# Kernel optimization log

Hardware: AMD Instinct MI355X
Metric: run time of the kernel (lower is better)

The kernel has to match this reference:

```python
import jax, jax.numpy as jnp
import numpy as np

N_STUDENT = 100000
N_COURSE = 20000
N_EDGES = 1000000
HIDDEN = 128


def setup_inputs() -> dict:
    key = jax.random.key(0)
    ks = jax.random.split(key, 8)
    scale = 1.0 / np.sqrt(2 * HIDDEN)
    return {
        "z_student": jax.random.normal(ks[0], (N_STUDENT, HIDDEN), dtype=jnp.float32),
        "z_course": jax.random.normal(ks[1], (N_COURSE, HIDDEN), dtype=jnp.float32),
        "row": jax.random.randint(ks[2], (N_EDGES,), 0, N_STUDENT, dtype=jnp.int64),
        "col": jax.random.randint(ks[3], (N_EDGES,), 0, N_COURSE, dtype=jnp.int64),
        "W1": jax.random.normal(ks[4], (2 * HIDDEN, HIDDEN), dtype=jnp.float32) * scale,
        "b1": jnp.zeros((HIDDEN,), dtype=jnp.float32),
        "W2": jax.random.normal(ks[5], (HIDDEN, 1), dtype=jnp.float32) * (1.0 / np.sqrt(HIDDEN)),
        "b2": jnp.zeros((1,), dtype=jnp.float32),
    }


def reference(z_student, z_course, row, col, W1, b1, W2, b2):
    # gather endpoint embeddings and concat along feature dim: [E, 2H]
    z = jnp.concatenate([z_student[row], z_course[col]], axis=-1)
    h = jax.nn.relu(z @ W1 + b1)   # [E, H]
    out = h @ W2 + b2              # [E, 1]
    return out.reshape(-1)
```

## Files before the change

kernel.cpp:

```cpp
#include <hip/hip_runtime.h>
#include <hip/hip_bf16.h>
#include <hip/hip_fp16.h>


typedef _Float16 half2v __attribute__((ext_vector_type(2)));
typedef _Float16 half8v __attribute__((ext_vector_type(8)));
typedef __fp16   fp16x2 __attribute__((ext_vector_type(2)));
typedef float    float4v __attribute__((ext_vector_type(4)));

__global__ __launch_bounds__(256) void conv_w(const float* __restrict__ W1,
                                              const float* __restrict__ W2,
                                              _Float16* __restrict__ Wt,
                                              _Float16* __restrict__ w2h) {
    int b = blockIdx.x, t = threadIdx.x;
    if (b == 8) { if (t < 128) w2h[t] = (_Float16)W2[t]; return; }
    __shared__ _Float16 lds[32][136];
    int h = b >> 2, n0 = (b & 3) * 32;
    for (int i = 0; i < 16; ++i) {
        int idx = i * 256 + t;
        int k = idx >> 5, nn = idx & 31;
        lds[nn][k] = (_Float16)W1[(h * 128 + k) * 128 + n0 + nn];
    }
    __syncthreads();
    for (int j = 0; j < 2; ++j) {
        int idx = j * 256 + t;
        int nn = idx >> 4, kc = idx & 15;
        half8v v;
        #pragma unroll
        for (int q = 0; q < 8; ++q) v[q] = lds[nn][kc * 8 + q];
        *(half8v*)&Wt[((h * 128 + n0 + nn) * 128) + kc * 8] = v;
    }
}

__global__ __launch_bounds__(256) void gemm_u(
    const float* __restrict__ Zs, const float* __restrict__ Zc,
    const _Float16* __restrict__ Wt, const float* __restrict__ b1,
    _Float16* __restrict__ Us, _Float16* __restrict__ Uc,
    int Ms, int Mc, int nbs)
{
    __shared__ uint4 ldsW[2048];
    const int bid = blockIdx.x, t = threadIdx.x;

    const float* Z; _Float16* U; const _Float16* W; int M, m0, addB;
    if (bid < nbs) { Z = Zs; U = Us; M = Ms; m0 = bid * 64;         W = Wt;         addB = 1; }
    else           { Z = Zc; U = Uc; M = Mc; m0 = (bid - nbs) * 64; W = Wt + 16384; addB = 0; }

    const uint4* Wv = (const uint4*)W;
    #pragma unroll
    for (int i = 0; i < 8; ++i) {
        int j = i * 256 + t;
        int n = j >> 4, ch = j & 15;
        ldsW[n * 16 + (ch ^ ((n >> 3) & 7))] = Wv[j];
    }
    __syncthreads();

    const int wave = t >> 6, lane = t & 63, quad = lane >> 4, l16 = lane & 15;
    int mrow = m0 + wave * 16 + l16;
    int mload = mrow < M ? mrow : M - 1;
    const float* zrow = Z + (long)mload * 128;

    float4v acc[8];
    #pragma unroll
    for (int nt = 0; nt < 8; ++nt) acc[nt] = (float4v)(0.0f);

    #pragma unroll
    for (int c = 0; c < 4; ++c) {
        const float4v* pa = (const float4v*)(zrow + c * 32 + quad * 8);
        float4v a0 = pa[0], a1 = pa[1];
        fp16x2 p[4];
        p[0] = __builtin_amdgcn_cvt_pkrtz(a0[0], a0[1]);
        p[1] = __builtin_amdgcn_cvt_pkrtz(a0[2], a0[3]);
        p[2] = __builtin_amdgcn_cvt_pkrtz(a1[0], a1[1]);
        p[3] = __builtin_amdgcn_cvt_pkrtz(a1[2], a1[3]);
        half8v af;
        __builtin_memcpy(&af, &p[0], 16);
        const int ch = c * 4 + quad;
        #pragma unroll
        for (int nt = 0; nt < 8; ++nt) {
            const int n = l16 * 8 + nt;
            const half8v* pb = (const half8v*)&ldsW[n * 16 + (ch ^ (l16 & 7))];
            acc[nt] = __builtin_amdgcn_mfma_f32_16x16x32_f16(af, *pb, acc[nt], 0, 0, 0);
        }
    }

    float bv[8];
    if (addB) {
        const float4v* pb1 = (const float4v*)(b1 + l16 * 8);
        float4v x0 = pb1[0], x1 = pb1[1];
        bv[0]=x0[0]; bv[1]=x0[1]; bv[2]=x0[2]; bv[3]=x0[3];
        bv[4]=x1[0]; bv[5]=x1[1]; bv[6]=x1[2]; bv[7]=x1[3];
    } else {
        #pragma unroll
        for (int i = 0; i < 8; ++i) bv[i] = 0.0f;
    }

    const int rbase = m0 + wave * 16 + quad * 4;
    #pragma unroll
    for (int r = 0; r < 4; ++r) {
        int rr = rbase + r;
        if (rr < M) {
            half8v o;
            #pragma unroll
            for (int nt = 0; nt < 8; ++nt) o[nt] = (_Float16)(acc[nt][r] + bv[nt]);
            *(half8v*)&U[(long)rr * 128 + l16 * 8] = o;
        }
    }
}

__global__ __launch_bounds__(256) void edge_kernel(
    const int* __restrict__ row, const int* __restrict__ col,
    const _Float16* __restrict__ us, const _Float16* __restrict__ uc,
    const _Float16* __restrict__ w2h, const float* __restrict__ b2,
    float* __restrict__ out, int E)
{
    const int t = threadIdx.x;
    const int sub = t & 7;
    long e = (long)blockIdx.x * 32 + (t >> 3);
    if (e >= E) return;
    int r = row[e], c = col[e];

    const uint4* pa = (const uint4*)(us  + (long)r * 128 + sub * 16);
    const uint4* pb = (const uint4*)(uc  + (long)c * 128 + sub * 16);
    const uint4* pw = (const uint4*)(w2h + sub * 16);
    uint4 a0 = pa[0], a1 = pa[1];
    uint4 c0 = pb[0], c1 = pb[1];
    uint4 w0 = pw[0], w1 = pw[1];

    half2v A[8], B[8], W[8];
    *(uint4*)&A[0] = a0; *(uint4*)&A[4] = a1;
    *(uint4*)&B[0] = c0; *(uint4*)&B[4] = c1;
    *(uint4*)&W[0] = w0; *(uint4*)&W[4] = w1;

    const half2v zero = {(_Float16)0, (_Float16)0};
    float s = 0.0f;
    #pragma unroll
    for (int i = 0; i < 8; ++i) {
        half2v h = A[i] + B[i];
        h = __builtin_elementwise_max(h, zero);
        s += (float)h[0] * (float)W[i][0];
        s += (float)h[1] * (float)W[i][1];
    }
    s += __shfl_xor(s, 1);
    s += __shfl_xor(s, 2);
    s += __shfl_xor(s, 4);
    if (sub == 0) out[e] = s + b2[0];
}

extern "C" void kernel_launch(void* const* d_in, const int* in_sizes, int n_in,
                              void* d_out, int out_size, void* d_ws, size_t ws_size,
                              hipStream_t stream) {
    const float* zs  = (const float*)d_in[0];
    const float* zc  = (const float*)d_in[1];
    const int*   row = (const int*)d_in[2];
    const int*   col = (const int*)d_in[3];
    const float* W1  = (const float*)d_in[4];
    const float* b1  = (const float*)d_in[5];
    const float* W2  = (const float*)d_in[6];
    const float* b2  = (const float*)d_in[7];
    float* out = (float*)d_out;

    const int Ms = in_sizes[0] / 128;
    const int Mc = in_sizes[1] / 128;
    const int E  = in_sizes[2];

    _Float16* Wt  = (_Float16*)d_ws;
    _Float16* w2h = (_Float16*)((char*)d_ws + 65536);
    _Float16* us  = (_Float16*)((char*)d_ws + 65536 + 256);
    _Float16* uc  = us + (size_t)Ms * 128;

    const int nbs = (Ms + 63) / 64, nbc = (Mc + 63) / 64;

    conv_w<<<9, 256, 0, stream>>>(W1, W2, Wt, w2h);
    gemm_u<<<nbs + nbc, 256, 0, stream>>>(zs, zc, Wt, b1, us, uc, Ms, Mc, nbs);
    edge_kernel<<<(E + 31) / 32, 256, 0, stream>>>(row, col, us, uc, w2h, b2, out, E);
}
```

Before: 170.3 us.

## Bucket edges by student row range to localize gathers, then unscatter outputs

Adds a pass that sorts edges into 16 buckets by student row range, a bucketed edge kernel whose blocks each work within one row range, and an unscatter pass that writes results back in the original edge order. The aim is to improve cache locality of the 25.6 MB fp16 student table gathers by keeping each bucket's working set near L2 size. In exchange it costs extra passes and traffic for row/col/pos/outB (tens of MB), plus a slow scalar fallback for edges that overflow a bucket's capacity. Interleaving bucket IDs across blocks means all buckets run concurrently, which may undercut the locality gain.

```diff
diff --git a/kernel.cpp b/kernel.cpp
--- a/kernel.cpp
+++ b/kernel.cpp
@@ -8,12 +8,20 @@
 typedef __fp16   fp16x2 __attribute__((ext_vector_type(2)));
 typedef float    float4v __attribute__((ext_vector_type(4)));
 
+#define NB  16
+#define CAP 70000
+
 __global__ __launch_bounds__(256) void conv_w(const float* __restrict__ W1,
                                               const float* __restrict__ W2,
                                               _Float16* __restrict__ Wt,
-                                              _Float16* __restrict__ w2h) {
+                                              _Float16* __restrict__ w2h,
+                                              int* __restrict__ cnt) {
     int b = blockIdx.x, t = threadIdx.x;
-    if (b == 8) { if (t < 128) w2h[t] = (_Float16)W2[t]; return; }
+    if (b == 8) {
+        if (t < 128) w2h[t] = (_Float16)W2[t];
+        if (t < 32)  cnt[t] = 0;
+        return;
+    }
     __shared__ _Float16 lds[32][136];
     int h = b >> 2, n0 = (b & 3) * 32;
     for (int i = 0; i < 16; ++i) {
@@ -107,6 +115,124 @@
     }
 }
 
+__global__ __launch_bounds__(256) void bucket_scatter(
+    const int* __restrict__ row, const int* __restrict__ col,
+    int* __restrict__ rB, int* __restrict__ cB, int* __restrict__ pos,
+    int* __restrict__ cnt, int E, float scale)
+{
+    __shared__ int hist[NB], base[NB], hist2[NB];
+    const int t = threadIdx.x;
+    if (t < NB) { hist[t] = 0; hist2[t] = 0; }
+    __syncthreads();
+    const long e0 = (long)blockIdx.x * 1024 + t;
+    int r[4], c[4], bk[4];
+    bool v[4];
+    #pragma unroll
+    for (int k = 0; k < 4; ++k) {
+        long e = e0 + k * 256;
+        v[k] = e < (long)E;
+        long ee = v[k] ? e : 0;
+        r[k] = __builtin_nontemporal_load(&row[ee]);
+        c[k] = __builtin_nontemporal_load(&col[ee]);
+        int b = (int)((float)r[k] * scale);
+        bk[k] = b > NB - 1 ? NB - 1 : b;
+        if (v[k]) atomicAdd(&hist[bk[k]], 1);
+    }
+    __syncthreads();
+    if (t < NB) base[t] = atomicAdd(&cnt[t], hist[t]);
+    __syncthreads();
+    #pragma unroll
+    for (int k = 0; k < 4; ++k) {
+        if (!v[k]) continue;
+        int o = atomicAdd(&hist2[bk[k]], 1);
+        int slot = base[bk[k]] + o;
+        long e = e0 + k * 256;
+        if (slot < CAP) {
+            int g = bk[k] * CAP + slot;
+            rB[g] = r[k];
+            cB[g] = c[k];
+            __builtin_nontemporal_store(g, &pos[e]);
+        } else {
+            __builtin_nontemporal_store(-1, &pos[e]);
+        }
+    }
+}
+
+__global__ __launch_bounds__(256) void edge_bucket(
+    const int* __restrict__ rB, const int* __restrict__ cB,
+    const int* __restrict__ cnt,
+    const _Float16* __restrict__ us, const _Float16* __restrict__ uc,
+    const _Float16* __restrict__ w2h, const float* __restrict__ b2,
+    float* __restrict__ outB)
+{
+    const int t = threadIdx.x, sub = t & 7;
+    const int b = blockIdx.x & (NB - 1);
+    const int j = blockIdx.x >> 4;
+    int n = cnt[b]; n = n < CAP ? n : CAP;
+    const int seg = b * CAP;
+
+    const uint4* pw = (const uint4*)(w2h + sub * 16);
+    uint4 w0 = pw[0], w1 = pw[1];
+    half2v W[8];
+    *(uint4*)&W[0] = w0; *(uint4*)&W[4] = w1;
+    const float bb = b2[0];
+    const half2v zero = {(_Float16)0, (_Float16)0};
+
+    for (int i0 = j * 32; i0 < n; i0 += 128 * 32) {
+        int i = i0 + (t >> 3);
+        bool act = i < n;
+        int ii = act ? i : n - 1;
+        int r = __builtin_nontemporal_load(&rB[seg + ii]);
+        int c = __builtin_nontemporal_load(&cB[seg + ii]);
+        const uint4* pa = (const uint4*)(us + (long)r * 128 + sub * 16);
+        const uint4* pb = (const uint4*)(uc + (long)c * 128 + sub * 16);
+        uint4 a0 = pa[0], a1 = pa[1];
+        uint4 c0 = pb[0], c1 = pb[1];
+        half2v A[8], B[8];
+        *(uint4*)&A[0] = a0; *(uint4*)&A[4] = a1;
+        *(uint4*)&B[0] = c0; *(uint4*)&B[4] = c1;
+        float s = 0.0f;
+        #pragma unroll
+        for (int q = 0; q < 8; ++q) {
+            half2v h = A[q] + B[q];
+            h = __builtin_elementwise_max(h, zero);
+            s += (float)h[0] * (float)W[q][0];
+            s += (float)h[1] * (float)W[q][1];
+        }
+        s += __shfl_xor(s, 1);
+        s += __shfl_xor(s, 2);
+        s += __shfl_xor(s, 4);
+        if (sub == 0 && act) outB[seg + i] = s + bb;
+    }
+}
+
+__global__ __launch_bounds__(256) void unscatter(
+    const int* __restrict__ pos, const float* __restrict__ outB,
+    const int* __restrict__ row, const int* __restrict__ col,
+    const _Float16* __restrict__ us, const _Float16* __restrict__ uc,
+    const _Float16* __restrict__ w2h, const float* __restrict__ b2,
+    float* __restrict__ out, int E)
+{
+    const int t = threadIdx.x;
+    #pragma unroll
+    for (int k = 0; k < 4; ++k) {
+        long e = (long)blockIdx.x * 1024 + k * 256 + t;
+        if (e >= (long)E) return;
+        int p = pos[e];
+        if (p >= 0) {
+            __builtin_nontemporal_store(outB[p], &out[e]);
+        } else {
+            int r = row[e], c = col[e];
+            float s = b2[0];
+            for (int kk = 0; kk < 128; ++kk) {
+                float h = (float)us[(long)r * 128 + kk] + (float)uc[(long)c * 128 + kk];
+                s += fmaxf(h, 0.0f) * (float)w2h[kk];
+            }
+            out[e] = s;
+        }
+    }
+}
+
 __global__ __launch_bounds__(256) void edge_kernel(
     const int* __restrict__ row, const int* __restrict__ col,
     const _Float16* __restrict__ us, const _Float16* __restrict__ uc,
@@ -163,14 +289,31 @@
     const int Mc = in_sizes[1] / 128;
     const int E  = in_sizes[2];
 
-    _Float16* Wt  = (_Float16*)d_ws;
-    _Float16* w2h = (_Float16*)((char*)d_ws + 65536);
-    _Float16* us  = (_Float16*)((char*)d_ws + 65536 + 256);
-    _Float16* uc  = us + (size_t)Ms * 128;
+    char* wsb = (char*)d_ws;
+    _Float16* Wt  = (_Float16*)wsb;
+    _Float16* w2h = (_Float16*)(wsb + 65536);
+    int*      cnt = (int*)(wsb + 65792);
+    size_t off = 66048;
+    _Float16* us = (_Float16*)(wsb + off);  off += (size_t)Ms * 256;
+    _Float16* uc = (_Float16*)(wsb + off);  off += (size_t)Mc * 256;
+    int* rB    = (int*)(wsb + off);  off += (size_t)NB * CAP * 4;
+    int* cB    = (int*)(wsb + off);  off += (size_t)NB * CAP * 4;
+    int* pos   = (int*)(wsb + off);  off += (size_t)E * 4;
+    float* outB = (float*)(wsb + off); off += (size_t)NB * CAP * 4;
+    const bool bucketed = (off <= ws_size);
 
     const int nbs = (Ms + 63) / 64, nbc = (Mc + 63) / 64;
 
-    conv_w<<<9, 256, 0, stream>>>(W1, W2, Wt, w2h);
+    conv_w<<<9, 256, 0, stream>>>(W1, W2, Wt, w2h, cnt);
     gemm_u<<<nbs + nbc, 256, 0, stream>>>(zs, zc, Wt, b1, us, uc, Ms, Mc, nbs);
-    edge_kernel<<<(E + 31) / 32, 256, 0, stream>>>(row, col, us, uc, w2h, b2, out, E);
-}
+    if (bucketed) {
+        bucket_scatter<<<(E + 1023) / 1024, 256, 0, stream>>>(
+            row, col, rB, cB, pos, cnt, E, (float)NB / (float)Ms);
+        edge_bucket<<<NB * 128, 256, 0, stream>>>(rB, cB, cnt, us, uc, w2h, b2, outB);
+        unscatter<<<(E + 1023) / 1024, 256, 0, stream>>>(
+            pos, outB, row, col, us, uc, w2h, b2, out, E);
+    } else {
+        edge_kernel<<<(E + 31) / 32, 256, 0, stream>>>(row, col, us, uc, w2h, b2, out, E);
+    }
+    (void)n_in; (void)out_size;
+}
```

New measurement: 182.9 us. +7.4%, slower.
